# Optimization experiments

Measured on AMD Instinct MI355X. Metric: run time of the kernel, lower is better.

## Reference

```python
import jax, jax.numpy as jnp
import numpy as np
from jax import lax

# TT-conv configuration (matches init_kwargs)
M = (4, 8, 8)        # in_c_modes, prod = 256
O = (4, 8, 8)        # out_c_modes, prod = 256
R = (16, 16, 16, 1)  # ranks with trailing 1 appended as in the module
B, H, W = 8, 64, 64
IN_C = int(np.prod(M))


def setup_inputs() -> dict:
    key = jax.random.key(0)
    ks = jax.random.split(key, 6)
    X = jax.random.normal(ks[0], (B, IN_C, H, W), jnp.float32)
    conv_w = jax.random.normal(ks[1], (R[0], 1, 3, 3), jnp.float32) * 0.3
    conv_b = jax.random.normal(ks[2], (R[0],), jnp.float32) * 0.05
    def xavier(k, shape):
        fan_in, fan_out = shape[1], shape[0]
        std = (2.0 / (fan_in + fan_out)) ** 0.5
        return jax.random.normal(k, shape, jnp.float32) * std
    core1 = xavier(ks[3], (O[0] * R[1], R[0] * M[0]))  # (64, 64)
    core2 = xavier(ks[4], (O[1] * R[2], R[1] * M[1]))  # (128, 128)
    core3 = xavier(ks[5], (O[2] * R[3], R[2] * M[2]))  # (8, 128)
    return {"X": X, "conv_w": conv_w, "conv_b": conv_b,
            "core1": core1, "core2": core2, "core3": core3}


def reference(X, conv_w, conv_b, core1, core2, core3):
    b, in_c, h, w = X.shape
    # core0: depth-agnostic 1->r0 conv applied per input channel
    y = lax.conv_general_dilated(
        X.reshape(-1, 1, h, w), conv_w,
        window_strides=(1, 1), padding=((1, 1), (1, 1)),
        dimension_numbers=("NCHW", "OIHW", "NCHW"))
    y = y + conv_b[None, :, None, None]          # (B*in_c, r0, h, w)
    hh, ww = y.shape[-2:]
    # (B, m1, m2, m3, r0, h, w): in_c factored row-major, m1 most significant
    y = y.reshape(b, M[0], M[1], M[2], R[0], hh, ww)
    # TT cores reshaped (o_i, r_{i+1}, r_i, m_i)
    G1 = core1.reshape(O[0], R[1], R[0], M[0])
    G2 = core2.reshape(O[1], R[2], R[1], M[1])
    G3 = core3.reshape(O[2], R[3], R[2], M[2])
    # Full TT contraction chain collapsed into one einsum; s (=r3) has size 1.
    out = jnp.einsum("bijkrhw,auri,cvuj,dsvk->bacdhw",
                     y, G1, G2, G3, optimize=True)
    # channel order (o1, o2, o3) with o3 fastest, as in the torch module
    return out.reshape(b, O[0] * O[1] * O[2], hh, ww)
```

## Files before the change

### kernel.cpp

```cpp
#include <hip/hip_runtime.h>
#include <hip/hip_bf16.h>
#include <stdint.h>

typedef __attribute__((ext_vector_type(8))) short short8;
typedef __attribute__((ext_vector_type(4))) float f32x4;

#define XP_BYTES   17842176
#define XP_PAD     1024
#define OFF_W9     (XP_BYTES + XP_PAD)
#define W9_BYTES   (8*9*256*32*2)
#define OFF_BIAS   (OFF_W9 + W9_BYTES)

__device__ __forceinline__ short f2bf(float f) {
  __hip_bfloat16 h = __float2bfloat16(f);
  return *reinterpret_cast<short*>(&h);
}

__device__ __forceinline__ void gl_lds16(const void* g, void* l) {
  __builtin_amdgcn_global_load_lds(
      (const __attribute__((address_space(1))) void*)g,
      (__attribute__((address_space(3))) void*)l, 16, 0, 0);
}

__global__ void k_weights(const float* __restrict__ core1,
                          const float* __restrict__ core2,
                          const float* __restrict__ core3,
                          const float* __restrict__ convw,
                          const float* __restrict__ convb,
                          short* __restrict__ W9, float* __restrict__ bias) {
  __shared__ float H2s[1024];
  __shared__ float red[256];
  const int o = blockIdx.x, c = threadIdx.x;
  const int a = o >> 6, c2 = (o >> 3) & 7, d = o & 7;
#pragma unroll
  for (int p = 0; p < 4; ++p) {
    int idx = c + (p << 8);
    int k = idx & 7, j = (idx >> 3) & 7, u = idx >> 6;
    float s = 0.f;
#pragma unroll
    for (int v = 0; v < 16; ++v)
      s += core2[(c2 * 16 + v) * 128 + u * 8 + j] * core3[d * 128 + v * 8 + k];
    H2s[idx] = s;
  }
  __syncthreads();
  const int i = c >> 6, j = (c >> 3) & 7, k = c & 7;
  float Wr[16];
#pragma unroll
  for (int r = 0; r < 16; ++r) Wr[r] = 0.f;
  for (int u = 0; u < 16; ++u) {
    float h = H2s[u * 64 + j * 8 + k];
    const float* c1 = core1 + (a * 16 + u) * 64 + i;
#pragma unroll
    for (int r = 0; r < 16; ++r) Wr[r] += c1[r * 4] * h;
  }
  const int cb = c >> 5, cl = c & 31, g = cl >> 3, pos = cl & 7;
  const int gslot = g ^ (o & 3);
#pragma unroll
  for (int t = 0; t < 9; ++t) {
    float s = 0.f;
#pragma unroll
    for (int r = 0; r < 16; ++r) s += Wr[r] * convw[r * 9 + t];
    W9[((size_t)((cb * 9 + t) * 256 + o)) * 32 + gslot * 8 + pos] = f2bf(s);
  }
  float s = 0.f;
#pragma unroll
  for (int r = 0; r < 16; ++r) s += Wr[r] * convb[r];
  red[c] = s;
  __syncthreads();
  for (int st = 128; st > 0; st >>= 1) {
    if (c < st) red[c] += red[c + st];
    __syncthreads();
  }
  if (c == 0) bias[o] = red[0];
}

__global__ void k_pad(const float* __restrict__ X, short* __restrict__ Xp) {
  const int y = blockIdx.x, b = blockIdx.y, cb = blockIdx.z;
  const int t = threadIdx.x;
  const int x = t & 63, sub = t >> 6;
  const int xp = x + 1, yp = y + 1;
  const int gslot = sub ^ (xp & 3);
  const float* src = X + ((size_t)(b * 256 + cb * 32 + sub * 8) * 64 + y) * 64 + x;
  short8 v;
#pragma unroll
  for (int k = 0; k < 8; ++k) v[k] = f2bf(src[(size_t)k * 4096]);
  const size_t granule = ((size_t)((b * 8 + cb) * 66 + yp) * 66 + xp) * 4 + gslot;
  *(short8*)(Xp + granule * 8) = v;
}

__global__ __launch_bounds__(256, 2) void k_gemm(
    const short* __restrict__ Xp, const short* __restrict__ W9,
    const float* __restrict__ bias, float* __restrict__ out) {
  __shared__ __align__(16) short XL[12800];
  __shared__ __align__(16) short WL[18432];

  const int tid  = threadIdx.x;
  const int lane = tid & 63;
  const int wv   = tid >> 6;
  const int l15  = lane & 15;
  const int gl   = lane >> 4;
  const int h0    = blockIdx.x << 2;
  const int oBase = blockIdx.y << 6;
  const int b     = blockIdx.z;

  f32x4 acc[4][4];
#pragma unroll
  for (int io = 0; io < 4; ++io)
#pragma unroll
    for (int ip = 0; ip < 4; ++ip)
      acc[io][ip] = (f32x4){0.f, 0.f, 0.f, 0.f};

  for (int cb = 0; cb < 8; ++cb) {
    __syncthreads();
#pragma unroll 1
    for (int q = wv; q < 36; q += 4) {
      const int t = q >> 2, sub = q & 3;
      const short* g = W9 +
          (((size_t)(((cb * 9 + t) << 8) + oBase + (sub << 4))) << 5) + (lane << 3);
      gl_lds16(g, &WL[((t << 6) + (sub << 4)) << 5]);
    }
    const size_t xb = ((size_t)(((b << 3) + cb) * 66 + h0) * 66) << 5;
#pragma unroll 1
    for (int q = wv; q < 25; q += 4) {
      gl_lds16(Xp + xb + (q << 9) + (lane << 3), &XL[q << 9]);
    }
    __syncthreads();
#pragma unroll
    for (int t = 0; t < 9; ++t) {
      const int dy = t / 3, dx = t % 3;
      const int row = wv + dy;
      short8 af[4], bfr[4];
#pragma unroll
      for (int io = 0; io < 4; ++io) {
        const int ol = (io << 4) + l15;
        af[io] = *(const short8*)&WL[(((t << 6) + ol) << 5) + ((gl ^ (ol & 3)) << 3)];
      }
#pragma unroll
      for (int ip = 0; ip < 4; ++ip) {
        const int x = (ip << 4) + l15 + dx;
        bfr[ip] = *(const short8*)&XL[(((row * 66 + x) << 2) + (gl ^ (x & 3))) << 3];
      }
#pragma unroll
      for (int io = 0; io < 4; ++io)
#pragma unroll
        for (int ip = 0; ip < 4; ++ip)
          acc[io][ip] = __builtin_amdgcn_mfma_f32_16x16x32_bf16(
              af[io], bfr[ip], acc[io][ip], 0, 0, 0);
    }
  }

  const int h = h0 + wv;
#pragma unroll
  for (int io = 0; io < 4; ++io) {
#pragma unroll
    for (int r = 0; r < 4; ++r) {
      const int oG = oBase + (io << 4) + (gl << 2) + r;
      const float bv = bias[oG];
      float* op = out + (((size_t)((b << 8) + oG)) << 12) + (h << 6);
#pragma unroll
      for (int ip = 0; ip < 4; ++ip)
        op[(ip << 4) + l15] = acc[io][ip][r] + bv;
    }
  }
}

extern "C" void kernel_launch(void* const* d_in, const int* in_sizes, int n_in,
                              void* d_out, int out_size, void* d_ws, size_t ws_size,
                              hipStream_t stream) {
  (void)in_sizes; (void)n_in; (void)out_size; (void)ws_size;
  const float* X     = (const float*)d_in[0];
  const float* convw = (const float*)d_in[1];
  const float* convb = (const float*)d_in[2];
  const float* core1 = (const float*)d_in[3];
  const float* core2 = (const float*)d_in[4];
  const float* core3 = (const float*)d_in[5];
  float* out = (float*)d_out;
  char*  ws  = (char*)d_ws;

  short* Xp   = (short*)ws;
  short* W9   = (short*)(ws + OFF_W9);
  float* bias = (float*)(ws + OFF_BIAS);

  hipMemsetAsync(Xp, 0, XP_BYTES + XP_PAD, stream);
  k_weights<<<256, 256, 0, stream>>>(core1, core2, core3, convw, convb, W9, bias);
  k_pad    <<<dim3(64, 8, 8), 256, 0, stream>>>(X, Xp);
  k_gemm   <<<dim3(16, 4, 8), 256, 0, stream>>>(Xp, W9, bias, out);
}
```

Before: 139.9 us.

## Double-buffer LDS tiles, compute two rows per wave, fold padding into pad kernel

The GEMM kernel now handles 8 output rows per block, 2 per wave. Each weight fragment loaded from LDS feeds two rows of MFMAs, and input fragments are reused across the three dy taps. LDS staging is double-buffered so the next channel block's global-to-LDS copies are issued before the current one is computed. The pad kernel now writes the zero border itself, which removes the separate memset of the padded buffer. In exchange the grid is halved to 256 blocks at one block per CU with about 156 KB of LDS, which lowers occupancy and latency hiding.

```diff
diff --git a/kernel.cpp b/kernel.cpp
--- a/kernel.cpp
+++ b/kernel.cpp
@@ -75,91 +75,128 @@
 }
 
 __global__ void k_pad(const float* __restrict__ X, short* __restrict__ Xp) {
-  const int y = blockIdx.x, b = blockIdx.y, cb = blockIdx.z;
+  const int yp = blockIdx.x, b = blockIdx.y, cb = blockIdx.z;
   const int t = threadIdx.x;
   const int x = t & 63, sub = t >> 6;
-  const int xp = x + 1, yp = y + 1;
+  const size_t rowg = ((size_t)((b * 8 + cb) * 66 + yp)) * 264;
+  const short8 z = (short8){0, 0, 0, 0, 0, 0, 0, 0};
+  if (yp == 0 || yp == 65) {
+    *(short8*)(Xp + (rowg + (size_t)(x << 2) + sub) * 8) = z;
+    if (x < 2)
+      *(short8*)(Xp + (rowg + (size_t)((64 + x) << 2) + sub) * 8) = z;
+    return;
+  }
+  const int y = yp - 1, xp = x + 1;
   const int gslot = sub ^ (xp & 3);
   const float* src = X + ((size_t)(b * 256 + cb * 32 + sub * 8) * 64 + y) * 64 + x;
   short8 v;
 #pragma unroll
   for (int k = 0; k < 8; ++k) v[k] = f2bf(src[(size_t)k * 4096]);
-  const size_t granule = ((size_t)((b * 8 + cb) * 66 + yp) * 66 + xp) * 4 + gslot;
-  *(short8*)(Xp + granule * 8) = v;
-}
-
-__global__ __launch_bounds__(256, 2) void k_gemm(
+  *(short8*)(Xp + (rowg + (size_t)(xp << 2) + gslot) * 8) = v;
+  if (x < 2)
+    *(short8*)(Xp + (rowg + (size_t)((x * 65) << 2) + sub) * 8) = z;
+}
+
+__device__ __forceinline__ void stage_tiles(
+    const short* __restrict__ Xp, const short* __restrict__ W9,
+    short* XLd, short* WLd, int cb, int h0, int oBase, int b, int wv, int lane) {
+  const size_t xb = ((size_t)(((b << 3) + cb) * 66 + h0) * 66) << 5;
+#pragma unroll 1
+  for (int q = wv; q < 42; q += 4)
+    gl_lds16(Xp + xb + (q << 9) + (lane << 3), XLd + (q << 9));
+#pragma unroll 1
+  for (int q = wv; q < 36; q += 4) {
+    const int t = q >> 2, sub = q & 3;
+    const short* g = W9 +
+        (((size_t)(((cb * 9 + t) << 8) + oBase + (sub << 4))) << 5) + (lane << 3);
+    gl_lds16(g, WLd + (((t << 6) + (sub << 4)) << 5));
+  }
+}
+
+__global__ __launch_bounds__(256, 1) void k_gemm(
     const short* __restrict__ Xp, const short* __restrict__ W9,
     const float* __restrict__ bias, float* __restrict__ out) {
-  __shared__ __align__(16) short XL[12800];
-  __shared__ __align__(16) short WL[18432];
+  __shared__ __align__(16) short XL[2][21504];
+  __shared__ __align__(16) short WL[2][18432];
 
   const int tid  = threadIdx.x;
   const int lane = tid & 63;
   const int wv   = tid >> 6;
   const int l15  = lane & 15;
   const int gl   = lane >> 4;
-  const int h0    = blockIdx.x << 2;
+  const int h0    = blockIdx.x << 3;
   const int oBase = blockIdx.y << 6;
   const int b     = blockIdx.z;
-
-  f32x4 acc[4][4];
-#pragma unroll
-  for (int io = 0; io < 4; ++io)
-#pragma unroll
-    for (int ip = 0; ip < 4; ++ip)
-      acc[io][ip] = (f32x4){0.f, 0.f, 0.f, 0.f};
-
+  const int r0    = wv << 1;
+
+  f32x4 acc[2][4][4];
+#pragma unroll
+  for (int rr = 0; rr < 2; ++rr)
+#pragma unroll
+    for (int io = 0; io < 4; ++io)
+#pragma unroll
+      for (int ip = 0; ip < 4; ++ip)
+        acc[rr][io][ip] = (f32x4){0.f, 0.f, 0.f, 0.f};
+
+  stage_tiles(Xp, W9, &XL[0][0], &WL[0][0], 0, h0, oBase, b, wv, lane);
+
+  int cur = 0;
   for (int cb = 0; cb < 8; ++cb) {
     __syncthreads();
-#pragma unroll 1
-    for (int q = wv; q < 36; q += 4) {
-      const int t = q >> 2, sub = q & 3;
-      const short* g = W9 +
-          (((size_t)(((cb * 9 + t) << 8) + oBase + (sub << 4))) << 5) + (lane << 3);
-      gl_lds16(g, &WL[((t << 6) + (sub << 4)) << 5]);
+    if (cb < 7)
+      stage_tiles(Xp, W9, &XL[cur ^ 1][0], &WL[cur ^ 1][0],
+                  cb + 1, h0, oBase, b, wv, lane);
+    const short* XLc = &XL[cur][0];
+    const short* WLc = &WL[cur][0];
+#pragma unroll
+    for (int dx = 0; dx < 3; ++dx) {
+      short8 bfr[4][4];
+#pragma unroll
+      for (int xr = 0; xr < 4; ++xr) {
+        const int prow = r0 + xr;
+#pragma unroll
+        for (int ip = 0; ip < 4; ++ip) {
+          const int x = (ip << 4) + l15 + dx;
+          bfr[xr][ip] = *(const short8*)&XLc[(((prow * 66 + x) << 2) + (gl ^ (x & 3))) << 3];
+        }
+      }
+#pragma unroll
+      for (int dy = 0; dy < 3; ++dy) {
+        const int t = dy * 3 + dx;
+        short8 af[4];
+#pragma unroll
+        for (int io = 0; io < 4; ++io) {
+          const int ol = (io << 4) + l15;
+          af[io] = *(const short8*)&WLc[(((t << 6) + ol) << 5) + ((gl ^ (ol & 3)) << 3)];
+        }
+#pragma unroll
+        for (int io = 0; io < 4; ++io)
+#pragma unroll
+          for (int ip = 0; ip < 4; ++ip) {
+            acc[0][io][ip] = __builtin_amdgcn_mfma_f32_16x16x32_bf16(
+                af[io], bfr[dy][ip], acc[0][io][ip], 0, 0, 0);
+            acc[1][io][ip] = __builtin_amdgcn_mfma_f32_16x16x32_bf16(
+                af[io], bfr[dy + 1][ip], acc[1][io][ip], 0, 0, 0);
+          }
+      }
     }
-    const size_t xb = ((size_t)(((b << 3) + cb) * 66 + h0) * 66) << 5;
-#pragma unroll 1
-    for (int q = wv; q < 25; q += 4) {
-      gl_lds16(Xp + xb + (q << 9) + (lane << 3), &XL[q << 9]);
-    }
-    __syncthreads();
-#pragma unroll
-    for (int t = 0; t < 9; ++t) {
-      const int dy = t / 3, dx = t % 3;
-      const int row = wv + dy;
-      short8 af[4], bfr[4];
-#pragma unroll
-      for (int io = 0; io < 4; ++io) {
-        const int ol = (io << 4) + l15;
-        af[io] = *(const short8*)&WL[(((t << 6) + ol) << 5) + ((gl ^ (ol & 3)) << 3)];
+    cur ^= 1;
+  }
+
+#pragma unroll
+  for (int rr = 0; rr < 2; ++rr) {
+    const int h = h0 + r0 + rr;
+#pragma unroll
+    for (int io = 0; io < 4; ++io) {
+#pragma unroll
+      for (int r = 0; r < 4; ++r) {
+        const int oG = oBase + (io << 4) + (gl << 2) + r;
+        const float bv = bias[oG];
+        float* op = out + (((size_t)((b << 8) + oG)) << 12) + (h << 6);
+#pragma unroll
+        for (int ip = 0; ip < 4; ++ip)
+          op[(ip << 4) + l15] = acc[rr][io][ip][r] + bv;
       }
-#pragma unroll
-      for (int ip = 0; ip < 4; ++ip) {
-        const int x = (ip << 4) + l15 + dx;
-        bfr[ip] = *(const short8*)&XL[(((row * 66 + x) << 2) + (gl ^ (x & 3))) << 3];
-      }
-#pragma unroll
-      for (int io = 0; io < 4; ++io)
-#pragma unroll
-        for (int ip = 0; ip < 4; ++ip)
-          acc[io][ip] = __builtin_amdgcn_mfma_f32_16x16x32_bf16(
-              af[io], bfr[ip], acc[io][ip], 0, 0, 0);
-    }
-  }
-
-  const int h = h0 + wv;
-#pragma unroll
-  for (int io = 0; io < 4; ++io) {
-#pragma unroll
-    for (int r = 0; r < 4; ++r) {
-      const int oG = oBase + (io << 4) + (gl << 2) + r;
-      const float bv = bias[oG];
-      float* op = out + (((size_t)((b << 8) + oG)) << 12) + (h << 6);
-#pragma unroll
-      for (int ip = 0; ip < 4; ++ip)
-        op[(ip << 4) + l15] = acc[io][ip][r] + bv;
     }
   }
 }
@@ -181,8 +218,7 @@
   short* W9   = (short*)(ws + OFF_W9);
   float* bias = (float*)(ws + OFF_BIAS);
 
-  hipMemsetAsync(Xp, 0, XP_BYTES + XP_PAD, stream);
   k_weights<<<256, 256, 0, stream>>>(core1, core2, core3, convw, convb, W9, bias);
-  k_pad    <<<dim3(64, 8, 8), 256, 0, stream>>>(X, Xp);
-  k_gemm   <<<dim3(16, 4, 8), 256, 0, stream>>>(Xp, W9, bias, out);
-}
+  k_pad    <<<dim3(66, 8, 8), 256, 0, stream>>>(X, Xp);
+  k_gemm   <<<dim3(8, 4, 8), 256, 0, stream>>>(Xp, W9, bias, out);
+}
```

After: 138.6 us. No clear change (-1.0%).
